# Kernel tuning notes

Hardware: AMD Instinct MI355X
Metric: run time of the kernel (lower is better)

## Reference

```python
import jax, jax.numpy as jnp
import numpy as np

WINDOW_SIZE = 256

def setup_inputs() -> dict:
    key = jax.random.key(0)
    kq, kk, kv = jax.random.split(key, 3)
    B, H, S, D = 1, 16, 4096, 64
    return {
        "query": jax.random.normal(kq, (B, H, S, D), dtype=jnp.float32),
        "key": jax.random.normal(kk, (B, H, S, D), dtype=jnp.float32),
        "value": jax.random.normal(kv, (B, H, S, D), dtype=jnp.float32),
    }

def reference(query, key, value):
    # Faithful to the torch module: dense QK^T, banded mask with -1e9 fill,
    # softmax over full row, then AV. Returns (output, attention_weights).
    d_k = query.shape[-1]
    S = query.shape[2]
    scores = jnp.einsum("bhqd,bhkd->bhqk", query, key) / jnp.sqrt(jnp.float32(d_k))
    idx = jnp.arange(S)
    band = jnp.abs(idx[:, None] - idx[None, :]) <= WINDOW_SIZE  # [S, S]
    scores = jnp.where(band[None, None, :, :], scores, jnp.float32(-1e9))
    attn = jax.nn.softmax(scores, axis=-1)
    out = jnp.einsum("bhqk,bhkd->bhqd", attn, value)
    return (out, attn)
```

## Files before the change

### kernel.cpp

```cpp
#include <hip/hip_runtime.h>
#include <math.h>

#define S_LEN 4096
#define D_DIM 64
#define H_NUM 16
#define WIN   256
#define TQ    16
#define NCH   9
#define KSTR  72
#define PBSTR 584

typedef __attribute__((ext_vector_type(8))) short          bf16x8;
typedef __attribute__((ext_vector_type(4))) float          f32x4;
typedef __attribute__((ext_vector_type(8))) unsigned short u16x8;
typedef __attribute__((ext_vector_type(4))) unsigned short u16x4;

static __device__ __forceinline__ unsigned short f2bf(float x) {
    unsigned int u = __float_as_uint(x);
    u = (u + 0x7FFFu + ((u >> 16) & 1u)) >> 16;
    return (unsigned short)u;
}
static __device__ __forceinline__ float bf2f(unsigned short h) {
    return __uint_as_float(((unsigned int)h) << 16);
}

__global__ __launch_bounds__(256) void swa_kernel(
    const float* __restrict__ Q,
    const float* __restrict__ K,
    const float* __restrict__ V,
    float* __restrict__ out,
    float* __restrict__ attn)
{
    const int tid = threadIdx.x;
    const int q0  = blockIdx.x * TQ;
    const int h   = blockIdx.y;

    const float* __restrict__ Qh = Q + (size_t)h * S_LEN * D_DIM;
    const float* __restrict__ Kh = K + (size_t)h * S_LEN * D_DIM;
    const float* __restrict__ Vh = V + (size_t)h * S_LEN * D_DIM;

    __shared__ unsigned short qbf[TQ * KSTR];
    __shared__ unsigned short kvb[64 * KSTR];
    __shared__ unsigned short pbf[TQ * PBSTR];
    __shared__ float red[64];
    __shared__ float linv[TQ];

    const int k0   = max(q0 - WIN, 0);
    const int lane = tid & 63;
    const int wv   = tid >> 6;
    const int quad = lane >> 4;
    const int n16  = lane & 15;

    {
        const int row = tid >> 4, c4 = (tid & 15) * 4;
        const float4 v = *(const float4*)(Qh + (size_t)(q0 + row) * D_DIM + c4);
        u16x4 p; p.x = f2bf(v.x); p.y = f2bf(v.y); p.z = f2bf(v.z); p.w = f2bf(v.w);
        *(u16x4*)&qbf[row * KSTR + c4] = p;
    }
    __syncthreads();

    const bf16x8 aq0 = *(const bf16x8*)&qbf[n16 * KSTR + quad * 8];
    const bf16x8 aq1 = *(const bf16x8*)&qbf[n16 * KSTR + 32 + quad * 8];

    float psum[4] = {0.f, 0.f, 0.f, 0.f};
    #pragma unroll
    for (int c = 0; c < NCH; ++c) {
        const int kb = k0 + c * 64;
        {
            const int key = tid >> 2, d0 = (tid & 3) * 16;
            const int kg  = min(kb + key, S_LEN - 1);
            const float4* s4 = (const float4*)(Kh + (size_t)kg * D_DIM + d0);
            const float4 x0 = s4[0], x1 = s4[1], x2 = s4[2], x3 = s4[3];
            u16x8 p0, p1;
            p0[0]=f2bf(x0.x); p0[1]=f2bf(x0.y); p0[2]=f2bf(x0.z); p0[3]=f2bf(x0.w);
            p0[4]=f2bf(x1.x); p0[5]=f2bf(x1.y); p0[6]=f2bf(x1.z); p0[7]=f2bf(x1.w);
            p1[0]=f2bf(x2.x); p1[1]=f2bf(x2.y); p1[2]=f2bf(x2.z); p1[3]=f2bf(x2.w);
            p1[4]=f2bf(x3.x); p1[5]=f2bf(x3.y); p1[6]=f2bf(x3.z); p1[7]=f2bf(x3.w);
            *(u16x8*)&kvb[key * KSTR + d0]     = p0;
            *(u16x8*)&kvb[key * KSTR + d0 + 8] = p1;
        }
        __syncthreads();

        const bf16x8 b0 = *(const bf16x8*)&kvb[(wv * 16 + n16) * KSTR + quad * 8];
        const bf16x8 b1 = *(const bf16x8*)&kvb[(wv * 16 + n16) * KSTR + 32 + quad * 8];
        f32x4 acc = {0.f, 0.f, 0.f, 0.f};
        acc = __builtin_amdgcn_mfma_f32_16x16x32_bf16(aq0, b0, acc, 0, 0, 0);
        acc = __builtin_amdgcn_mfma_f32_16x16x32_bf16(aq1, b1, acc, 0, 0, 0);

        const int key_abs = kb + wv * 16 + n16;
        #pragma unroll
        for (int r = 0; r < 4; ++r) {
            const int qrow  = quad * 4 + r;
            const int q_abs = q0 + qrow;
            const bool in   = (key_abs < S_LEN) &&
                              (key_abs >= q_abs - WIN) && (key_abs <= q_abs + WIN);
            const float e = in ? __expf(acc[r] * 0.125f) : 0.f;
            pbf[qrow * PBSTR + c * 64 + wv * 16 + n16] = f2bf(e);
            psum[r] += e;
        }
        __syncthreads();
    }

    #pragma unroll
    for (int r = 0; r < 4; ++r) {
        float s = psum[r];
        s += __shfl_down(s, 8, 16);
        s += __shfl_down(s, 4, 16);
        s += __shfl_down(s, 2, 16);
        s += __shfl_down(s, 1, 16);
        if (n16 == 0) red[wv * 16 + quad * 4 + r] = s;
    }
    __syncthreads();
    if (tid < TQ)
        linv[tid] = 1.f / (red[tid] + red[16 + tid] + red[32 + tid] + red[48 + tid]);
    __syncthreads();

    f32x4 oacc = {0.f, 0.f, 0.f, 0.f};
    const int dd = wv * 16 + n16;
    const int sd = ((dd >> 4) + (dd & 7)) & 7;
    #pragma unroll
    for (int c = 0; c < NCH; ++c) {
        const int kb = k0 + c * 64;
        {
            const int key = tid >> 2, d0 = (tid & 3) * 16;
            const int kg  = min(kb + key, S_LEN - 1);
            const float4* s4 = (const float4*)(Vh + (size_t)kg * D_DIM + d0);
            const float4 y0 = s4[0], y1 = s4[1], y2 = s4[2], y3 = s4[3];
            const float vals[16] = {y0.x,y0.y,y0.z,y0.w, y1.x,y1.y,y1.z,y1.w,
                                    y2.x,y2.y,y2.z,y2.w, y3.x,y3.y,y3.z,y3.w};
            #pragma unroll
            for (int jj = 0; jj < 16; ++jj) {
                const int d  = d0 + jj;
                const int sw = ((d >> 4) + (d & 7)) & 7;
                kvb[d * 64 + (key ^ (sw * 8))] = f2bf(vals[jj]);
            }
        }
        __syncthreads();

        const bf16x8 pa0 = *(const bf16x8*)&pbf[n16 * PBSTR + c * 64 + quad * 8];
        const bf16x8 pa1 = *(const bf16x8*)&pbf[n16 * PBSTR + c * 64 + 32 + quad * 8];
        const bf16x8 vb0 = *(const bf16x8*)&kvb[dd * 64 + 8 * (quad ^ sd)];
        const bf16x8 vb1 = *(const bf16x8*)&kvb[dd * 64 + 8 * ((4 + quad) ^ sd)];
        oacc = __builtin_amdgcn_mfma_f32_16x16x32_bf16(pa0, vb0, oacc, 0, 0, 0);
        oacc = __builtin_amdgcn_mfma_f32_16x16x32_bf16(pa1, vb1, oacc, 0, 0, 0);
        __syncthreads();
    }
    #pragma unroll
    for (int r = 0; r < 4; ++r) {
        const int qrow = quad * 4 + r;
        out[((size_t)h * S_LEN + q0 + qrow) * D_DIM + dd] = oacc[r] * linv[qrow];
    }

    for (int qq = 0; qq < TQ; ++qq) {
        const int qa  = q0 + qq;
        const int b0q = max(qa - WIN, 0);
        const int b1q = min(qa + WIN, S_LEN - 1);
        const float qi = linv[qq];
        f32x4* arow = (f32x4*)(attn + ((size_t)h * S_LEN + qa) * S_LEN);
        const unsigned short* prow = &pbf[qq * PBSTR];
        for (int j4 = tid; j4 < S_LEN / 4; j4 += 256) {
            const int j = j4 * 4;
            f32x4 w = {0.f, 0.f, 0.f, 0.f};
            if (j >= b0q && j + 3 <= b1q) {
                const u16x4 p = *(const u16x4*)&prow[j - k0];
                w[0] = bf2f(p.x) * qi; w[1] = bf2f(p.y) * qi;
                w[2] = bf2f(p.z) * qi; w[3] = bf2f(p.w) * qi;
            } else if (j + 3 >= b0q && j <= b1q) {
                #pragma unroll
                for (int e = 0; e < 4; ++e) {
                    const int jj = j + e;
                    if (jj >= b0q && jj <= b1q) w[e] = bf2f(prow[jj - k0]) * qi;
                }
            }
            __builtin_nontemporal_store(w, &arow[j4]);
        }
    }
}

extern "C" void kernel_launch(void* const* d_in, const int* in_sizes, int n_in,
                              void* d_out, int out_size, void* d_ws, size_t ws_size,
                              hipStream_t stream) {
    const float* Q = (const float*)d_in[0];
    const float* K = (const float*)d_in[1];
    const float* V = (const float*)d_in[2];
    float* out  = (float*)d_out;
    float* attn = out + (size_t)H_NUM * S_LEN * D_DIM;

    dim3 grid(S_LEN / TQ, H_NUM);
    swa_kernel<<<grid, 256, 0, stream>>>(Q, K, V, out, attn);
}
```

Measured before the change: 1.120 ms.

## Double query tile to 32 rows and prefetch K/V chunks into registers

Each block now handles 32 query rows split into two 16-row MFMA sub-tiles that share each loaded K/V chunk. This halves the number of blocks and the redundant K/V global loads and bf16 conversions across overlapping windows. The next K and V chunks are now loaded into registers while the current chunk is being computed, so global load latency can overlap with MFMA work. In exchange, LDS use roughly doubles for the probability buffer and register pressure rises, which may lower occupancy in the write-dominated attn store phase.

```diff
diff --git a/kernel.cpp b/kernel.cpp
--- a/kernel.cpp
+++ b/kernel.cpp
@@ -5,7 +5,7 @@
 #define D_DIM 64
 #define H_NUM 16
 #define WIN   256
-#define TQ    16
+#define TQ    32
 #define NCH   9
 #define KSTR  72
 #define PBSTR 584
@@ -42,7 +42,7 @@
     __shared__ unsigned short qbf[TQ * KSTR];
     __shared__ unsigned short kvb[64 * KSTR];
     __shared__ unsigned short pbf[TQ * PBSTR];
-    __shared__ float red[64];
+    __shared__ float red[4 * TQ];
     __shared__ float linv[TQ];
 
     const int k0   = max(q0 - WIN, 0);
@@ -51,104 +51,139 @@
     const int quad = lane >> 4;
     const int n16  = lane & 15;
 
+    const int skey = tid >> 2, sd0 = (tid & 3) * 16;
+
+    float4 kx0, kx1, kx2, kx3;
     {
-        const int row = tid >> 4, c4 = (tid & 15) * 4;
-        const float4 v = *(const float4*)(Qh + (size_t)(q0 + row) * D_DIM + c4);
-        u16x4 p; p.x = f2bf(v.x); p.y = f2bf(v.y); p.z = f2bf(v.z); p.w = f2bf(v.w);
-        *(u16x4*)&qbf[row * KSTR + c4] = p;
+        const int kg = min(k0 + skey, S_LEN - 1);
+        const float4* s4 = (const float4*)(Kh + (size_t)kg * D_DIM + sd0);
+        kx0 = s4[0]; kx1 = s4[1]; kx2 = s4[2]; kx3 = s4[3];
+    }
+
+    {
+        const int row = tid >> 3, c8 = (tid & 7) * 8;
+        const float4 v0 = *(const float4*)(Qh + (size_t)(q0 + row) * D_DIM + c8);
+        const float4 v1 = *(const float4*)(Qh + (size_t)(q0 + row) * D_DIM + c8 + 4);
+        u16x8 p;
+        p[0]=f2bf(v0.x); p[1]=f2bf(v0.y); p[2]=f2bf(v0.z); p[3]=f2bf(v0.w);
+        p[4]=f2bf(v1.x); p[5]=f2bf(v1.y); p[6]=f2bf(v1.z); p[7]=f2bf(v1.w);
+        *(u16x8*)&qbf[row * KSTR + c8] = p;
     }
     __syncthreads();
 
-    const bf16x8 aq0 = *(const bf16x8*)&qbf[n16 * KSTR + quad * 8];
-    const bf16x8 aq1 = *(const bf16x8*)&qbf[n16 * KSTR + 32 + quad * 8];
-
-    float psum[4] = {0.f, 0.f, 0.f, 0.f};
+    bf16x8 aqf[2][2];
+    #pragma unroll
+    for (int qt = 0; qt < 2; ++qt) {
+        aqf[qt][0] = *(const bf16x8*)&qbf[(qt * 16 + n16) * KSTR + quad * 8];
+        aqf[qt][1] = *(const bf16x8*)&qbf[(qt * 16 + n16) * KSTR + 32 + quad * 8];
+    }
+
+    float psum[8] = {0.f,0.f,0.f,0.f,0.f,0.f,0.f,0.f};
     #pragma unroll
     for (int c = 0; c < NCH; ++c) {
         const int kb = k0 + c * 64;
         {
-            const int key = tid >> 2, d0 = (tid & 3) * 16;
-            const int kg  = min(kb + key, S_LEN - 1);
-            const float4* s4 = (const float4*)(Kh + (size_t)kg * D_DIM + d0);
-            const float4 x0 = s4[0], x1 = s4[1], x2 = s4[2], x3 = s4[3];
             u16x8 p0, p1;
-            p0[0]=f2bf(x0.x); p0[1]=f2bf(x0.y); p0[2]=f2bf(x0.z); p0[3]=f2bf(x0.w);
-            p0[4]=f2bf(x1.x); p0[5]=f2bf(x1.y); p0[6]=f2bf(x1.z); p0[7]=f2bf(x1.w);
-            p1[0]=f2bf(x2.x); p1[1]=f2bf(x2.y); p1[2]=f2bf(x2.z); p1[3]=f2bf(x2.w);
-            p1[4]=f2bf(x3.x); p1[5]=f2bf(x3.y); p1[6]=f2bf(x3.z); p1[7]=f2bf(x3.w);
-            *(u16x8*)&kvb[key * KSTR + d0]     = p0;
-            *(u16x8*)&kvb[key * KSTR + d0 + 8] = p1;
-        }
-        __syncthreads();
+            p0[0]=f2bf(kx0.x); p0[1]=f2bf(kx0.y); p0[2]=f2bf(kx0.z); p0[3]=f2bf(kx0.w);
+            p0[4]=f2bf(kx1.x); p0[5]=f2bf(kx1.y); p0[6]=f2bf(kx1.z); p0[7]=f2bf(kx1.w);
+            p1[0]=f2bf(kx2.x); p1[1]=f2bf(kx2.y); p1[2]=f2bf(kx2.z); p1[3]=f2bf(kx2.w);
+            p1[4]=f2bf(kx3.x); p1[5]=f2bf(kx3.y); p1[6]=f2bf(kx3.z); p1[7]=f2bf(kx3.w);
+            *(u16x8*)&kvb[skey * KSTR + sd0]     = p0;
+            *(u16x8*)&kvb[skey * KSTR + sd0 + 8] = p1;
+        }
+        __syncthreads();
+
+        if (c + 1 < NCH) {
+            const int kg = min(kb + 64 + skey, S_LEN - 1);
+            const float4* s4 = (const float4*)(Kh + (size_t)kg * D_DIM + sd0);
+            kx0 = s4[0]; kx1 = s4[1]; kx2 = s4[2]; kx3 = s4[3];
+        }
 
         const bf16x8 b0 = *(const bf16x8*)&kvb[(wv * 16 + n16) * KSTR + quad * 8];
         const bf16x8 b1 = *(const bf16x8*)&kvb[(wv * 16 + n16) * KSTR + 32 + quad * 8];
-        f32x4 acc = {0.f, 0.f, 0.f, 0.f};
-        acc = __builtin_amdgcn_mfma_f32_16x16x32_bf16(aq0, b0, acc, 0, 0, 0);
-        acc = __builtin_amdgcn_mfma_f32_16x16x32_bf16(aq1, b1, acc, 0, 0, 0);
-
         const int key_abs = kb + wv * 16 + n16;
         #pragma unroll
-        for (int r = 0; r < 4; ++r) {
-            const int qrow  = quad * 4 + r;
-            const int q_abs = q0 + qrow;
-            const bool in   = (key_abs < S_LEN) &&
-                              (key_abs >= q_abs - WIN) && (key_abs <= q_abs + WIN);
-            const float e = in ? __expf(acc[r] * 0.125f) : 0.f;
-            pbf[qrow * PBSTR + c * 64 + wv * 16 + n16] = f2bf(e);
-            psum[r] += e;
-        }
-        __syncthreads();
-    }
-
-    #pragma unroll
-    for (int r = 0; r < 4; ++r) {
-        float s = psum[r];
+        for (int qt = 0; qt < 2; ++qt) {
+            f32x4 acc = {0.f, 0.f, 0.f, 0.f};
+            acc = __builtin_amdgcn_mfma_f32_16x16x32_bf16(aqf[qt][0], b0, acc, 0, 0, 0);
+            acc = __builtin_amdgcn_mfma_f32_16x16x32_bf16(aqf[qt][1], b1, acc, 0, 0, 0);
+
+            #pragma unroll
+            for (int r = 0; r < 4; ++r) {
+                const int qrow  = qt * 16 + quad * 4 + r;
+                const int q_abs = q0 + qrow;
+                const bool in   = (key_abs < S_LEN) &&
+                                  (key_abs >= q_abs - WIN) && (key_abs <= q_abs + WIN);
+                const float e = in ? __expf(acc[r] * 0.125f) : 0.f;
+                pbf[qrow * PBSTR + c * 64 + wv * 16 + n16] = f2bf(e);
+                psum[qt * 4 + r] += e;
+            }
+        }
+        __syncthreads();
+    }
+
+    float4 vx0, vx1, vx2, vx3;
+    {
+        const int kg = min(k0 + skey, S_LEN - 1);
+        const float4* s4 = (const float4*)(Vh + (size_t)kg * D_DIM + sd0);
+        vx0 = s4[0]; vx1 = s4[1]; vx2 = s4[2]; vx3 = s4[3];
+    }
+
+    #pragma unroll
+    for (int i = 0; i < 8; ++i) {
+        float s = psum[i];
         s += __shfl_down(s, 8, 16);
         s += __shfl_down(s, 4, 16);
         s += __shfl_down(s, 2, 16);
         s += __shfl_down(s, 1, 16);
-        if (n16 == 0) red[wv * 16 + quad * 4 + r] = s;
+        if (n16 == 0) red[wv * TQ + (i >> 2) * 16 + quad * 4 + (i & 3)] = s;
     }
     __syncthreads();
     if (tid < TQ)
-        linv[tid] = 1.f / (red[tid] + red[16 + tid] + red[32 + tid] + red[48 + tid]);
+        linv[tid] = 1.f / (red[tid] + red[TQ + tid] + red[2 * TQ + tid] + red[3 * TQ + tid]);
     __syncthreads();
 
-    f32x4 oacc = {0.f, 0.f, 0.f, 0.f};
+    f32x4 oacc0 = {0.f, 0.f, 0.f, 0.f};
+    f32x4 oacc1 = {0.f, 0.f, 0.f, 0.f};
     const int dd = wv * 16 + n16;
     const int sd = ((dd >> 4) + (dd & 7)) & 7;
     #pragma unroll
     for (int c = 0; c < NCH; ++c) {
-        const int kb = k0 + c * 64;
         {
-            const int key = tid >> 2, d0 = (tid & 3) * 16;
-            const int kg  = min(kb + key, S_LEN - 1);
-            const float4* s4 = (const float4*)(Vh + (size_t)kg * D_DIM + d0);
-            const float4 y0 = s4[0], y1 = s4[1], y2 = s4[2], y3 = s4[3];
-            const float vals[16] = {y0.x,y0.y,y0.z,y0.w, y1.x,y1.y,y1.z,y1.w,
-                                    y2.x,y2.y,y2.z,y2.w, y3.x,y3.y,y3.z,y3.w};
+            const float vals[16] = {vx0.x,vx0.y,vx0.z,vx0.w, vx1.x,vx1.y,vx1.z,vx1.w,
+                                    vx2.x,vx2.y,vx2.z,vx2.w, vx3.x,vx3.y,vx3.z,vx3.w};
             #pragma unroll
             for (int jj = 0; jj < 16; ++jj) {
-                const int d  = d0 + jj;
+                const int d  = sd0 + jj;
                 const int sw = ((d >> 4) + (d & 7)) & 7;
-                kvb[d * 64 + (key ^ (sw * 8))] = f2bf(vals[jj]);
+                kvb[d * 64 + (skey ^ (sw * 8))] = f2bf(vals[jj]);
             }
         }
         __syncthreads();
 
-        const bf16x8 pa0 = *(const bf16x8*)&pbf[n16 * PBSTR + c * 64 + quad * 8];
-        const bf16x8 pa1 = *(const bf16x8*)&pbf[n16 * PBSTR + c * 64 + 32 + quad * 8];
+        if (c + 1 < NCH) {
+            const int kg = min(k0 + (c + 1) * 64 + skey, S_LEN - 1);
+            const float4* s4 = (const float4*)(Vh + (size_t)kg * D_DIM + sd0);
+            vx0 = s4[0]; vx1 = s4[1]; vx2 = s4[2]; vx3 = s4[3];
+        }
+
         const bf16x8 vb0 = *(const bf16x8*)&kvb[dd * 64 + 8 * (quad ^ sd)];
         const bf16x8 vb1 = *(const bf16x8*)&kvb[dd * 64 + 8 * ((4 + quad) ^ sd)];
-        oacc = __builtin_amdgcn_mfma_f32_16x16x32_bf16(pa0, vb0, oacc, 0, 0, 0);
-        oacc = __builtin_amdgcn_mfma_f32_16x16x32_bf16(pa1, vb1, oacc, 0, 0, 0);
+        const bf16x8 pa00 = *(const bf16x8*)&pbf[n16 * PBSTR + c * 64 + quad * 8];
+        const bf16x8 pa01 = *(const bf16x8*)&pbf[n16 * PBSTR + c * 64 + 32 + quad * 8];
+        const bf16x8 pa10 = *(const bf16x8*)&pbf[(16 + n16) * PBSTR + c * 64 + quad * 8];
+        const bf16x8 pa11 = *(const bf16x8*)&pbf[(16 + n16) * PBSTR + c * 64 + 32 + quad * 8];
+        oacc0 = __builtin_amdgcn_mfma_f32_16x16x32_bf16(pa00, vb0, oacc0, 0, 0, 0);
+        oacc0 = __builtin_amdgcn_mfma_f32_16x16x32_bf16(pa01, vb1, oacc0, 0, 0, 0);
+        oacc1 = __builtin_amdgcn_mfma_f32_16x16x32_bf16(pa10, vb0, oacc1, 0, 0, 0);
+        oacc1 = __builtin_amdgcn_mfma_f32_16x16x32_bf16(pa11, vb1, oacc1, 0, 0, 0);
         __syncthreads();
     }
     #pragma unroll
     for (int r = 0; r < 4; ++r) {
-        const int qrow = quad * 4 + r;
-        out[((size_t)h * S_LEN + q0 + qrow) * D_DIM + dd] = oacc[r] * linv[qrow];
+        const int qr = quad * 4 + r;
+        out[((size_t)h * S_LEN + q0 + qr) * D_DIM + dd]      = oacc0[r] * linv[qr];
+        out[((size_t)h * S_LEN + q0 + 16 + qr) * D_DIM + dd] = oacc1[r] * linv[16 + qr];
     }
 
     for (int qq = 0; qq < TQ; ++qq) {
```

Result: no change. 1.126 ms (+0.5%).
